# Kernel tuning notes

Measured on AMD Instinct MI355X. Metric: run time of the kernel, lower is better.

The kernel has to match this reference:

```python
import jax, jax.numpy as jnp
import numpy as np

N = 100000
E = 1200000
D_IN, D_HID, D_OUT = 64, 64, 32


def setup_inputs() -> dict:
    key = jax.random.key(0)
    ks = jax.random.split(key, 8)
    x = jax.random.normal(ks[0], (N, D_IN), dtype=jnp.float32)
    edge_index = jax.random.randint(ks[1], (2, E), 0, N, dtype=jnp.int64)
    s_in = 1.0 / np.sqrt(D_IN)
    s_hid = 1.0 / np.sqrt(D_HID)
    return {
        "x": x,
        "edge_index": edge_index,
        "W1_l": jax.random.normal(ks[2], (D_IN, D_HID), dtype=jnp.float32) * s_in,
        "W1_r": jax.random.normal(ks[3], (D_IN, D_HID), dtype=jnp.float32) * s_in,
        "b1": jnp.zeros((D_HID,), dtype=jnp.float32),
        "W2_l": jax.random.normal(ks[4], (D_HID, D_OUT), dtype=jnp.float32) * s_hid,
        "W2_r": jax.random.normal(ks[5], (D_HID, D_OUT), dtype=jnp.float32) * s_hid,
        "b2": jnp.zeros((D_OUT,), dtype=jnp.float32),
    }


def _sage_conv(h, src, dst, W_l, W_r, b, n_nodes):
    # mean aggregation of source features onto destination nodes
    summed = jax.ops.segment_sum(h[src], dst, num_segments=n_nodes)  # [N, d]
    deg = jax.ops.segment_sum(jnp.ones((src.shape[0],), h.dtype), dst,
                              num_segments=n_nodes)  # [N]
    mean = summed / jnp.maximum(deg, 1.0)[:, None]
    # PyG SAGEConv: lin_l(aggr) + lin_r(x); bias lives on lin_l
    return mean @ W_l + b + h @ W_r


def reference(x, edge_index, W1_l, W1_r, b1, W2_l, W2_r, b2):
    src, dst = edge_index[0], edge_index[1]
    n = x.shape[0]
    h = jax.nn.relu(_sage_conv(x, src, dst, W1_l, W1_r, b1, n))
    return _sage_conv(h, src, dst, W2_l, W2_r, b2, n)
```

## Files before the change

### kernel.cpp

```cpp
#include <hip/hip_runtime.h>
#include <hip/hip_bf16.h>


#define D1 64
#define NQ 256
#define SUBN 391
#define QCAP 5632
#define LCAP 11520
#define BE 5120

static __device__ __forceinline__ float bf2f(ushort u) {
    unsigned int x = ((unsigned int)u) << 16;
    return __uint_as_float(x);
}
static __device__ __forceinline__ ushort f2bf(float f) {
    union { __hip_bfloat16 b; ushort u; } cv;
    cv.b = __float2bfloat16(f);
    return cv.u;
}
static __device__ __forceinline__ float lo2f(unsigned u) {
    return __uint_as_float(u << 16);
}
static __device__ __forceinline__ float hi2f(unsigned u) {
    return __uint_as_float(u & 0xffff0000u);
}
static __device__ __forceinline__ unsigned packbf(float x, float y) {
    return (unsigned)f2bf(x) | ((unsigned)f2bf(y) << 16);
}


__global__ __launch_bounds__(256)
void compact_edges256(const int* __restrict__ src, const int* __restrict__ dst,
                      int* __restrict__ tail, int2* __restrict__ queue, int E) {
    __shared__ int hist[NQ];
    __shared__ int base[NQ];
    int tid = threadIdx.x;
    int e0 = blockIdx.x * BE;
    int e1 = min(E, e0 + BE);

    hist[tid] = 0;
    __syncthreads();
    for (int e = e0 + tid; e < e1; e += 256)
        atomicAdd(&hist[dst[e] / SUBN], 1);
    __syncthreads();
    base[tid] = atomicAdd(&tail[tid], hist[tid]);
    hist[tid] = 0;
    __syncthreads();
    for (int e = e0 + tid; e < e1; e += 256) {
        int d = dst[e];
        int s = src[e];
        int p = d / SUBN;
        int pos = base[p] + atomicAdd(&hist[p], 1);
        if (pos < QCAP) queue[(size_t)p * QCAP + pos] = make_int2(s, d);
    }
}


__global__ __launch_bounds__(256)
void csr_build_local(const int2* __restrict__ queue, const int* __restrict__ tail,
                     int2* __restrict__ info, int* __restrict__ nbr, int N) {
    __shared__ int lcnt[512];
    __shared__ int psum[256];
    __shared__ int lnbr[LCAP];
    int tid = threadIdx.x;
    int p = blockIdx.x;
    int lo = p * SUBN;
    int nt = min(tail[p], QCAP);
    const int2* q = queue + (size_t)p * QCAP;
    int gbase = p * LCAP;

    lcnt[tid] = 0; lcnt[tid + 256] = 0;
    __syncthreads();
    for (int e = tid; e < nt; e += 256)
        atomicAdd(&lcnt[q[e].y - lo], 1);
    __syncthreads();

    int d0 = lcnt[2 * tid], d1 = lcnt[2 * tid + 1];
    int p0 = (d0 + 15) & ~15, p1 = (d1 + 15) & ~15;
    int s = p0 + p1;
    psum[tid] = s;
    __syncthreads();
    for (int off = 1; off < 256; off <<= 1) {
        int a = (tid >= off) ? psum[tid - off] : 0;
        __syncthreads();
        psum[tid] += a;
        __syncthreads();
    }
    int st0 = psum[tid] - s;
    int st1 = st0 + p0;
    int ptot = psum[255];

    {
        int li = 2 * tid, n = lo + li;
        if (li < SUBN && n < N) info[n] = make_int2(gbase + st0, d0);
        lcnt[li] = st0;
        li = 2 * tid + 1; n = lo + li;
        if (li < SUBN && n < N) info[n] = make_int2(gbase + st1, d1);
        lcnt[li] = st1;
    }
    __syncthreads();

    for (int e = tid; e < nt; e += 256) {
        int2 pr = q[e];
        int pos = atomicAdd(&lcnt[pr.y - lo], 1);
        lnbr[pos] = pr.x;
    }
    __syncthreads();

    for (int j = st0 + d0; j < st0 + p0; ++j) lnbr[j] = N;
    for (int j = st1 + d1; j < st1 + p1; ++j) lnbr[j] = N;
    __syncthreads();

    for (int i = tid; i < ptot; i += 256)
        nbr[gbase + i] = lnbr[i];
}


__global__ __launch_bounds__(256)
void cvt_bf16_init(const float* __restrict__ in, ushort* __restrict__ xh,
                   ushort* __restrict__ y2l, int* __restrict__ tail,
                   int n4, int N) {
    int i = blockIdx.x * 256 + threadIdx.x;
    if (i < n4) {
        float4 v = *(const float4*)&in[(size_t)i * 4];
        ushort4 u;
        u.x = f2bf(v.x); u.y = f2bf(v.y); u.z = f2bf(v.z); u.w = f2bf(v.w);
        *(ushort4*)&xh[(size_t)i * 4] = u;
    }
    if (blockIdx.x == 0) tail[threadIdx.x] = 0;
    if (blockIdx.x == 1) {
        if (threadIdx.x < D1) xh[(size_t)N * D1 + threadIdx.x] = 0;
        if (threadIdx.x < 32) y2l[(size_t)N * 32 + threadIdx.x] = 0;
    }
}


#define ACC8(u) do { \
    a0 += lo2f((u).x); a1 += hi2f((u).x); \
    a2 += lo2f((u).y); a3 += hi2f((u).y); \
    a4 += lo2f((u).z); a5 += hi2f((u).z); \
    a6 += lo2f((u).w); a7 += hi2f((u).w); } while (0)

__global__ __launch_bounds__(256)
void gather_mean8(const ushort* __restrict__ feat,
                  const int2* __restrict__ info,
                  const int* __restrict__ nbr,
                  ushort* __restrict__ mean, int N) {
    int wid  = (blockIdx.x * 256 + threadIdx.x) >> 6;
    int lane = threadIdx.x & 63;
    if (wid >= N) return;
    int2 ii = info[wid];
    int deg = ii.y;
    int m8 = (deg + 7) & ~7;
    const int* nb = nbr + ii.x;
    int r = lane >> 3;
    int c = lane & 7;
    const uint4* f4 = (const uint4*)feat;

    float a0 = 0, a1 = 0, a2 = 0, a3 = 0, a4 = 0, a5 = 0, a6 = 0, a7 = 0;
    int i = 0;
    for (; i + 16 <= m8; i += 16) {
        int e0 = nb[i + r];
        int e1 = nb[i + 8 + r];
        uint4 u0 = f4[(size_t)e0 * 8 + c];
        uint4 u1 = f4[(size_t)e1 * 8 + c];
        ACC8(u0);
        ACC8(u1);
    }
    if (i < m8) {
        int e0 = nb[i + r];
        uint4 u0 = f4[(size_t)e0 * 8 + c];
        ACC8(u0);
    }

    a0 += __shfl_xor(a0, 8, 64); a0 += __shfl_xor(a0, 16, 64); a0 += __shfl_xor(a0, 32, 64);
    a1 += __shfl_xor(a1, 8, 64); a1 += __shfl_xor(a1, 16, 64); a1 += __shfl_xor(a1, 32, 64);
    a2 += __shfl_xor(a2, 8, 64); a2 += __shfl_xor(a2, 16, 64); a2 += __shfl_xor(a2, 32, 64);
    a3 += __shfl_xor(a3, 8, 64); a3 += __shfl_xor(a3, 16, 64); a3 += __shfl_xor(a3, 32, 64);
    a4 += __shfl_xor(a4, 8, 64); a4 += __shfl_xor(a4, 16, 64); a4 += __shfl_xor(a4, 32, 64);
    a5 += __shfl_xor(a5, 8, 64); a5 += __shfl_xor(a5, 16, 64); a5 += __shfl_xor(a5, 32, 64);
    a6 += __shfl_xor(a6, 8, 64); a6 += __shfl_xor(a6, 16, 64); a6 += __shfl_xor(a6, 32, 64);
    a7 += __shfl_xor(a7, 8, 64); a7 += __shfl_xor(a7, 16, 64); a7 += __shfl_xor(a7, 32, 64);

    if (r == 0) {
        float inv = 1.0f / fmaxf((float)deg, 1.0f);
        uint4 o;
        o.x = packbf(a0 * inv, a1 * inv);
        o.y = packbf(a2 * inv, a3 * inv);
        o.z = packbf(a4 * inv, a5 * inv);
        o.w = packbf(a6 * inv, a7 * inv);
        ((uint4*)mean)[(size_t)wid * 8 + c] = o;
    }
}


__global__ __launch_bounds__(256)
void gather_out(const ushort* __restrict__ y2l,
                const float* __restrict__ y2r,
                const float* __restrict__ b2,
                const int2* __restrict__ info,
                const int* __restrict__ nbr,
                float* __restrict__ outp, int N) {
    int wid  = (blockIdx.x * 256 + threadIdx.x) >> 6;
    int lane = threadIdx.x & 63;
    if (wid >= N) return;
    int2 ii = info[wid];
    int deg = ii.y;
    int m16 = (deg + 15) & ~15;
    const int* nb = nbr + ii.x;
    int r = lane >> 2;
    int c = lane & 3;
    const uint4* f4 = (const uint4*)y2l;

    float a0 = 0, a1 = 0, a2 = 0, a3 = 0, a4 = 0, a5 = 0, a6 = 0, a7 = 0;
    int i = 0;
    for (; i + 32 <= m16; i += 32) {
        int e0 = nb[i + r];
        int e1 = nb[i + 16 + r];
        uint4 u0 = f4[(size_t)e0 * 4 + c];
        uint4 u1 = f4[(size_t)e1 * 4 + c];
        ACC8(u0);
        ACC8(u1);
    }
    if (i < m16) {
        int e0 = nb[i + r];
        uint4 u0 = f4[(size_t)e0 * 4 + c];
        ACC8(u0);
    }

    a0 += __shfl_xor(a0, 4, 64); a0 += __shfl_xor(a0, 8, 64); a0 += __shfl_xor(a0, 16, 64); a0 += __shfl_xor(a0, 32, 64);
    a1 += __shfl_xor(a1, 4, 64); a1 += __shfl_xor(a1, 8, 64); a1 += __shfl_xor(a1, 16, 64); a1 += __shfl_xor(a1, 32, 64);
    a2 += __shfl_xor(a2, 4, 64); a2 += __shfl_xor(a2, 8, 64); a2 += __shfl_xor(a2, 16, 64); a2 += __shfl_xor(a2, 32, 64);
    a3 += __shfl_xor(a3, 4, 64); a3 += __shfl_xor(a3, 8, 64); a3 += __shfl_xor(a3, 16, 64); a3 += __shfl_xor(a3, 32, 64);
    a4 += __shfl_xor(a4, 4, 64); a4 += __shfl_xor(a4, 8, 64); a4 += __shfl_xor(a4, 16, 64); a4 += __shfl_xor(a4, 32, 64);
    a5 += __shfl_xor(a5, 4, 64); a5 += __shfl_xor(a5, 8, 64); a5 += __shfl_xor(a5, 16, 64); a5 += __shfl_xor(a5, 32, 64);
    a6 += __shfl_xor(a6, 4, 64); a6 += __shfl_xor(a6, 8, 64); a6 += __shfl_xor(a6, 16, 64); a6 += __shfl_xor(a6, 32, 64);
    a7 += __shfl_xor(a7, 4, 64); a7 += __shfl_xor(a7, 8, 64); a7 += __shfl_xor(a7, 16, 64); a7 += __shfl_xor(a7, 32, 64);

    if (r == 0) {
        float inv = 1.0f / fmaxf((float)deg, 1.0f);
        size_t o = (size_t)wid * 32 + c * 8;
        float4 r0 = *(const float4*)&y2r[o];
        float4 r1 = *(const float4*)&y2r[o + 4];
        float4 v0, v1;
        v0.x = fmaf(a0, inv, r0.x + b2[c * 8 + 0]);
        v0.y = fmaf(a1, inv, r0.y + b2[c * 8 + 1]);
        v0.z = fmaf(a2, inv, r0.z + b2[c * 8 + 2]);
        v0.w = fmaf(a3, inv, r0.w + b2[c * 8 + 3]);
        v1.x = fmaf(a4, inv, r1.x + b2[c * 8 + 4]);
        v1.y = fmaf(a5, inv, r1.y + b2[c * 8 + 5]);
        v1.z = fmaf(a6, inv, r1.z + b2[c * 8 + 6]);
        v1.w = fmaf(a7, inv, r1.w + b2[c * 8 + 7]);
        *(float4*)&outp[o] = v0;
        *(float4*)&outp[o + 4] = v1;
    }
}


#define TA_STRIDE 66

__global__ __launch_bounds__(256)
void dense_sage1(const ushort* __restrict__ Am,
                 const ushort* __restrict__ Ax,
                 const float* __restrict__ Wm,
                 const float* __restrict__ Wx,
                 const float* __restrict__ bias,
                 const float* __restrict__ W2l,
                 const float* __restrict__ W2r,
                 ushort* __restrict__ y2l,
                 float* __restrict__ y2r,
                 int N) {
    __shared__ char smraw[128 * TA_STRIDE * 2];
    ushort* ta = (ushort*)smraw;
    float*  to = (float*)smraw;
    float*  tA = (float*)smraw;
    float*  tB = ((float*)smraw) + 32 * 65;

    int tid  = threadIdx.x;
    int w    = tid >> 6;
    int lane = tid & 63;
    int n0 = blockIdx.x * 64;

    #pragma unroll
    for (int i = 0; i < 8; ++i) {
        int flat = i * 256 + tid;
        int row  = flat >> 4;
        int c4   = (flat & 15) * 4;
        const ushort* A = (row < 64) ? Am : Ax;
        int node = row & 63;
        int grow = n0 + node;
        ushort4 u = make_ushort4(0, 0, 0, 0);
        if (grow < N) u = *(const ushort4*)&A[(size_t)grow * D1 + c4];
        int kb = ((row < 64) ? 0 : 64) + c4;
        ta[(kb + 0) * TA_STRIDE + node] = u.x;
        ta[(kb + 1) * TA_STRIDE + node] = u.y;
        ta[(kb + 2) * TA_STRIDE + node] = u.z;
        ta[(kb + 3) * TA_STRIDE + node] = u.w;
    }
    __syncthreads();

    int jb = __builtin_amdgcn_readfirstlane(w * 16);
    float c[16];
    #pragma unroll
    for (int j = 0; j < 16; ++j) c[j] = bias[jb + j];

    #pragma unroll 4
    for (int k = 0; k < 64; ++k) {
        float a = bf2f(ta[k * TA_STRIDE + lane]);
        #pragma unroll
        for (int j = 0; j < 16; ++j)
            c[j] = fmaf(a, Wm[k * 64 + jb + j], c[j]);
    }
    #pragma unroll 4
    for (int k = 0; k < 64; ++k) {
        float a = bf2f(ta[(64 + k) * TA_STRIDE + lane]);
        #pragma unroll
        for (int j = 0; j < 16; ++j)
            c[j] = fmaf(a, Wx[k * 64 + jb + j], c[j]);
    }
    #pragma unroll
    for (int j = 0; j < 16; ++j) c[j] = fmaxf(c[j], 0.0f);

    __syncthreads();
    #pragma unroll
    for (int j = 0; j < 16; ++j) to[(jb + j) * 65 + lane] = c[j];
    __syncthreads();

    int jb2 = __builtin_amdgcn_readfirstlane(w * 8);
    float c2[8], c3[8];
    #pragma unroll
    for (int j = 0; j < 8; ++j) { c2[j] = 0.0f; c3[j] = 0.0f; }
    #pragma unroll 4
    for (int k = 0; k < 64; ++k) {
        float a = to[k * 65 + lane];
        #pragma unroll
        for (int j = 0; j < 8; ++j) {
            c2[j] = fmaf(a, W2l[k * 32 + jb2 + j], c2[j]);
            c3[j] = fmaf(a, W2r[k * 32 + jb2 + j], c3[j]);
        }
    }
    __syncthreads();
    #pragma unroll
    for (int j = 0; j < 8; ++j) {
        tA[(jb2 + j) * 65 + lane] = c2[j];
        tB[(jb2 + j) * 65 + lane] = c3[j];
    }
    __syncthreads();

    #pragma unroll
    for (int i = 0; i < 2; ++i) {
        int flat = i * 256 + tid;
        int node = flat >> 3;
        int q    = flat & 7;
        int grow = n0 + node;
        if (grow < N) {
            ushort4 u;
            u.x = f2bf(tA[(q * 4 + 0) * 65 + node]);
            u.y = f2bf(tA[(q * 4 + 1) * 65 + node]);
            u.z = f2bf(tA[(q * 4 + 2) * 65 + node]);
            u.w = f2bf(tA[(q * 4 + 3) * 65 + node]);
            *(ushort4*)&y2l[(size_t)grow * 32 + q * 4] = u;
        }
    }
    #pragma unroll
    for (int i = 0; i < 2; ++i) {
        int flat = i * 256 + tid;
        int node = flat >> 3;
        int q    = flat & 7;
        int grow = n0 + node;
        if (grow < N) {
            float4 v;
            v.x = tB[(q * 4 + 0) * 65 + node];
            v.y = tB[(q * 4 + 1) * 65 + node];
            v.z = tB[(q * 4 + 2) * 65 + node];
            v.w = tB[(q * 4 + 3) * 65 + node];
            *(float4*)&y2r[(size_t)grow * 32 + q * 4] = v;
        }
    }
}


extern "C" void kernel_launch(void* const* d_in, const int* in_sizes, int n_in,
                              void* d_out, int out_size, void* d_ws, size_t ws_size,
                              hipStream_t stream) {
    const float* x   = (const float*)d_in[0];
    const int*   ei  = (const int*)d_in[1];
    const float* W1l = (const float*)d_in[2];
    const float* W1r = (const float*)d_in[3];
    const float* b1  = (const float*)d_in[4];
    const float* W2l = (const float*)d_in[5];
    const float* W2r = (const float*)d_in[6];
    const float* b2  = (const float*)d_in[7];
    float* out = (float*)d_out;

    int N = in_sizes[0] / D1;
    int E = in_sizes[1] / 2;
    const int* src = ei;
    const int* dst = ei + E;

    char* ws = (char*)d_ws;
    auto alignup = [](size_t v) { return (v + 255) & ~(size_t)255; };
    size_t off = 0;
    int*    tail  = (int*)(ws + off);    off += alignup(NQ * 4);
    int2*   queue = (int2*)(ws + off);   off += alignup((size_t)NQ * QCAP * 8);
    int*    nbr   = (int*)(ws + off);    off += alignup((size_t)NQ * LCAP * 4);
    int2*   info  = (int2*)(ws + off);   off += alignup((size_t)N * 8);
    ushort* xh    = (ushort*)(ws + off); off += alignup((size_t)(N + 1) * D1 * 2);
    ushort* y2l   = (ushort*)(ws + off); off += alignup((size_t)(N + 1) * 32 * 2);
    float*  y2r   = (float*)(ws + off);  off += alignup((size_t)N * 32 * 4);
    ushort* mean1 = (ushort*)d_out;

    int gb = (N + 3) / 4;
    int db = (N + 63) / 64;
    int cb = ((N * D1 / 4) + 255) / 256;
    int ab = (E + BE - 1) / BE;

    cvt_bf16_init<<<cb, 256, 0, stream>>>(x, xh, y2l, tail, N * D1 / 4, N);
    compact_edges256<<<ab, 256, 0, stream>>>(src, dst, tail, queue, E);
    csr_build_local<<<NQ, 256, 0, stream>>>(queue, tail, info, nbr, N);

    gather_mean8<<<gb, 256, 0, stream>>>(xh, info, nbr, mean1, N);
    dense_sage1<<<db, 256, 0, stream>>>(mean1, xh, W1l, W1r, b1, W2l, W2r, y2l, y2r, N);
    gather_out<<<gb, 256, 0, stream>>>(y2l, y2r, b2, info, nbr, out, N);
}
```

Measured before the change: 156.7 us.

## Replace scalar FMA dense SAGE layers with bf16 MFMA matrix instructions

The fused dense kernel for layer-1 projection and layer-2 pre-projection now uses 16x16x32 bf16 MFMA instructions instead of per-lane scalar FMA loops. Weights are pre-converted to bf16 in a transposed, concatenated layout inside the existing conversion kernel. The hidden activation is staged per wave in shared memory as bf16, which removes block-wide syncs. The aim is to cut the ALU-bound dense compute, at the cost of extra bf16 rounding on the weights and hidden activations.

```diff
diff --git a/kernel.cpp b/kernel.cpp
--- a/kernel.cpp
+++ b/kernel.cpp
@@ -8,6 +8,9 @@
 #define QCAP 5632
 #define LCAP 11520
 #define BE 5120
+
+typedef __attribute__((ext_vector_type(8))) short bf16x8;
+typedef __attribute__((ext_vector_type(4))) float f32x4;
 
 static __device__ __forceinline__ float bf2f(ushort u) {
     unsigned int x = ((unsigned int)u) << 16;
@@ -119,6 +122,9 @@
 __global__ __launch_bounds__(256)
 void cvt_bf16_init(const float* __restrict__ in, ushort* __restrict__ xh,
                    ushort* __restrict__ y2l, int* __restrict__ tail,
+                   const float* __restrict__ W1l, const float* __restrict__ W1r,
+                   const float* __restrict__ W2l, const float* __restrict__ W2r,
+                   ushort* __restrict__ WB1, ushort* __restrict__ WB2,
                    int n4, int N) {
     int i = blockIdx.x * 256 + threadIdx.x;
     if (i < n4) {
@@ -131,6 +137,20 @@
     if (blockIdx.x == 1) {
         if (threadIdx.x < D1) xh[(size_t)N * D1 + threadIdx.x] = 0;
         if (threadIdx.x < 32) y2l[(size_t)N * 32 + threadIdx.x] = 0;
+    }
+    if (blockIdx.x == 2) {
+        for (int idx = threadIdx.x; idx < 64 * 128; idx += 256) {
+            int j = idx >> 7, k = idx & 127;
+            float v = (k < 64) ? W1l[k * 64 + j] : W1r[(k - 64) * 64 + j];
+            WB1[idx] = f2bf(v);
+        }
+    }
+    if (blockIdx.x == 3) {
+        for (int idx = threadIdx.x; idx < 64 * 64; idx += 256) {
+            int j2 = idx >> 6, k = idx & 63;
+            float v = (j2 < 32) ? W2l[k * 32 + j2] : W2r[k * 32 + (j2 - 32)];
+            WB2[idx] = f2bf(v);
+        }
     }
 }
 
@@ -257,124 +277,86 @@
 }
 
 
-#define TA_STRIDE 66
-
-__global__ __launch_bounds__(256)
-void dense_sage1(const ushort* __restrict__ Am,
-                 const ushort* __restrict__ Ax,
-                 const float* __restrict__ Wm,
-                 const float* __restrict__ Wx,
-                 const float* __restrict__ bias,
-                 const float* __restrict__ W2l,
-                 const float* __restrict__ W2r,
-                 ushort* __restrict__ y2l,
-                 float* __restrict__ y2r,
-                 int N) {
-    __shared__ char smraw[128 * TA_STRIDE * 2];
-    ushort* ta = (ushort*)smraw;
-    float*  to = (float*)smraw;
-    float*  tA = (float*)smraw;
-    float*  tB = ((float*)smraw) + 32 * 65;
-
+__global__ __launch_bounds__(256)
+void dense_mfma(const ushort* __restrict__ Am,
+                const ushort* __restrict__ Ax,
+                const ushort* __restrict__ WB1,
+                const ushort* __restrict__ WB2,
+                const float* __restrict__ b1,
+                ushort* __restrict__ y2l,
+                float* __restrict__ y2r,
+                int N) {
+    __shared__ ushort hl[4][16 * 72];
     int tid  = threadIdx.x;
     int w    = tid >> 6;
     int lane = tid & 63;
-    int n0 = blockIdx.x * 64;
-
-    #pragma unroll
-    for (int i = 0; i < 8; ++i) {
-        int flat = i * 256 + tid;
-        int row  = flat >> 4;
-        int c4   = (flat & 15) * 4;
-        const ushort* A = (row < 64) ? Am : Ax;
-        int node = row & 63;
-        int grow = n0 + node;
-        ushort4 u = make_ushort4(0, 0, 0, 0);
-        if (grow < N) u = *(const ushort4*)&A[(size_t)grow * D1 + c4];
-        int kb = ((row < 64) ? 0 : 64) + c4;
-        ta[(kb + 0) * TA_STRIDE + node] = u.x;
-        ta[(kb + 1) * TA_STRIDE + node] = u.y;
-        ta[(kb + 2) * TA_STRIDE + node] = u.z;
-        ta[(kb + 3) * TA_STRIDE + node] = u.w;
-    }
-    __syncthreads();
-
-    int jb = __builtin_amdgcn_readfirstlane(w * 16);
-    float c[16];
-    #pragma unroll
-    for (int j = 0; j < 16; ++j) c[j] = bias[jb + j];
-
-    #pragma unroll 4
-    for (int k = 0; k < 64; ++k) {
-        float a = bf2f(ta[k * TA_STRIDE + lane]);
+    int mrow = lane & 15;
+    int kg   = lane >> 4;
+    int nbase = blockIdx.x * 64 + w * 16;
+    int arow = min(nbase + mrow, N - 1);
+
+    bf16x8 a[4];
+    a[0] = *(const bf16x8*)&Am[(size_t)arow * 64 +      kg * 8];
+    a[1] = *(const bf16x8*)&Am[(size_t)arow * 64 + 32 + kg * 8];
+    a[2] = *(const bf16x8*)&Ax[(size_t)arow * 64 +      kg * 8];
+    a[3] = *(const bf16x8*)&Ax[(size_t)arow * 64 + 32 + kg * 8];
+
+    f32x4 acc[4];
+    #pragma unroll
+    for (int t = 0; t < 4; ++t) acc[t] = (f32x4){0.f, 0.f, 0.f, 0.f};
+
+    #pragma unroll
+    for (int s = 0; s < 4; ++s) {
         #pragma unroll
-        for (int j = 0; j < 16; ++j)
-            c[j] = fmaf(a, Wm[k * 64 + jb + j], c[j]);
-    }
-    #pragma unroll 4
-    for (int k = 0; k < 64; ++k) {
-        float a = bf2f(ta[(64 + k) * TA_STRIDE + lane]);
+        for (int t = 0; t < 4; ++t) {
+            bf16x8 b = *(const bf16x8*)&WB1[(size_t)(t * 16 + mrow) * 128 + s * 32 + kg * 8];
+            acc[t] = __builtin_amdgcn_mfma_f32_16x16x32_bf16(a[s], b, acc[t], 0, 0, 0);
+        }
+    }
+
+    #pragma unroll
+    for (int t = 0; t < 4; ++t) {
+        float bv = b1[t * 16 + mrow];
         #pragma unroll
-        for (int j = 0; j < 16; ++j)
-            c[j] = fmaf(a, Wx[k * 64 + jb + j], c[j]);
-    }
-    #pragma unroll
-    for (int j = 0; j < 16; ++j) c[j] = fmaxf(c[j], 0.0f);
-
-    __syncthreads();
-    #pragma unroll
-    for (int j = 0; j < 16; ++j) to[(jb + j) * 65 + lane] = c[j];
-    __syncthreads();
-
-    int jb2 = __builtin_amdgcn_readfirstlane(w * 8);
-    float c2[8], c3[8];
-    #pragma unroll
-    for (int j = 0; j < 8; ++j) { c2[j] = 0.0f; c3[j] = 0.0f; }
-    #pragma unroll 4
-    for (int k = 0; k < 64; ++k) {
-        float a = to[k * 65 + lane];
+        for (int r = 0; r < 4; ++r) {
+            float hv = fmaxf(acc[t][r] + bv, 0.0f);
+            hl[w][(kg * 4 + r) * 72 + t * 16 + mrow] = f2bf(hv);
+        }
+    }
+
+    bf16x8 a2[2];
+    a2[0] = *(const bf16x8*)&hl[w][mrow * 72 +      kg * 8];
+    a2[1] = *(const bf16x8*)&hl[w][mrow * 72 + 32 + kg * 8];
+
+    f32x4 acc2[4];
+    #pragma unroll
+    for (int t = 0; t < 4; ++t) acc2[t] = (f32x4){0.f, 0.f, 0.f, 0.f};
+
+    #pragma unroll
+    for (int s = 0; s < 2; ++s) {
         #pragma unroll
-        for (int j = 0; j < 8; ++j) {
-            c2[j] = fmaf(a, W2l[k * 32 + jb2 + j], c2[j]);
-            c3[j] = fmaf(a, W2r[k * 32 + jb2 + j], c3[j]);
-        }
-    }
-    __syncthreads();
-    #pragma unroll
-    for (int j = 0; j < 8; ++j) {
-        tA[(jb2 + j) * 65 + lane] = c2[j];
-        tB[(jb2 + j) * 65 + lane] = c3[j];
-    }
-    __syncthreads();
-
-    #pragma unroll
-    for (int i = 0; i < 2; ++i) {
-        int flat = i * 256 + tid;
-        int node = flat >> 3;
-        int q    = flat & 7;
-        int grow = n0 + node;
-        if (grow < N) {
-            ushort4 u;
-            u.x = f2bf(tA[(q * 4 + 0) * 65 + node]);
-            u.y = f2bf(tA[(q * 4 + 1) * 65 + node]);
-            u.z = f2bf(tA[(q * 4 + 2) * 65 + node]);
-            u.w = f2bf(tA[(q * 4 + 3) * 65 + node]);
-            *(ushort4*)&y2l[(size_t)grow * 32 + q * 4] = u;
-        }
-    }
-    #pragma unroll
-    for (int i = 0; i < 2; ++i) {
-        int flat = i * 256 + tid;
-        int node = flat >> 3;
-        int q    = flat & 7;
-        int grow = n0 + node;
-        if (grow < N) {
-            float4 v;
-            v.x = tB[(q * 4 + 0) * 65 + node];
-            v.y = tB[(q * 4 + 1) * 65 + node];
-            v.z = tB[(q * 4 + 2) * 65 + node];
-            v.w = tB[(q * 4 + 3) * 65 + node];
-            *(float4*)&y2r[(size_t)grow * 32 + q * 4] = v;
+        for (int t = 0; t < 4; ++t) {
+            bf16x8 b = *(const bf16x8*)&WB2[(size_t)(t * 16 + mrow) * 64 + s * 32 + kg * 8];
+            acc2[t] = __builtin_amdgcn_mfma_f32_16x16x32_bf16(a2[s], b, acc2[t], 0, 0, 0);
+        }
+    }
+
+    #pragma unroll
+    for (int t = 0; t < 2; ++t) {
+        #pragma unroll
+        for (int r = 0; r < 4; ++r) {
+            int grow = nbase + kg * 4 + r;
+            if (grow < N)
+                y2l[(size_t)grow * 32 + t * 16 + mrow] = f2bf(acc2[t][r]);
+        }
+    }
+    #pragma unroll
+    for (int t = 2; t < 4; ++t) {
+        #pragma unroll
+        for (int r = 0; r < 4; ++r) {
+            int grow = nbase + kg * 4 + r;
+            if (grow < N)
+                y2r[(size_t)grow * 32 + (t - 2) * 16 + mrow] = acc2[t][r];
         }
     }
 }
@@ -408,6 +390,8 @@
     ushort* xh    = (ushort*)(ws + off); off += alignup((size_t)(N + 1) * D1 * 2);
     ushort* y2l   = (ushort*)(ws + off); off += alignup((size_t)(N + 1) * 32 * 2);
     float*  y2r   = (float*)(ws + off);  off += alignup((size_t)N * 32 * 4);
+    ushort* WB1   = (ushort*)(ws + off); off += alignup(64 * 128 * 2);
+    ushort* WB2   = (ushort*)(ws + off); off += alignup(64 * 64 * 2);
     ushort* mean1 = (ushort*)d_out;
 
     int gb = (N + 3) / 4;
@@ -415,11 +399,13 @@
     int cb = ((N * D1 / 4) + 255) / 256;
     int ab = (E + BE - 1) / BE;
 
-    cvt_bf16_init<<<cb, 256, 0, stream>>>(x, xh, y2l, tail, N * D1 / 4, N);
+    cvt_bf16_init<<<cb, 256, 0, stream>>>(x, xh, y2l, tail,
+                                          W1l, W1r, W2l, W2r, WB1, WB2,
+                                          N * D1 / 4, N);
     compact_edges256<<<ab, 256, 0, stream>>>(src, dst, tail, queue, E);
     csr_build_local<<<NQ, 256, 0, stream>>>(queue, tail, info, nbr, N);
 
     gather_mean8<<<gb, 256, 0, stream>>>(xh, info, nbr, mean1, N);
-    dense_sage1<<<db, 256, 0, stream>>>(mean1, xh, W1l, W1r, b1, W2l, W2r, y2l, y2r, N);
+    dense_mfma<<<db, 256, 0, stream>>>(mean1, xh, WB1, WB2, b1, y2l, y2r, N);
     gather_out<<<gb, 256, 0, stream>>>(y2l, y2r, b2, info, nbr, out, N);
 }
```

Measured after the change: 142.3 us. 9.2% less time.
